# Kernel optimization log

Measured on AMD Instinct MI355X. Metric: run time of the kernel, lower is better.

The kernel has to match this reference:

```python
import jax, jax.numpy as jnp
import numpy as np

N, T, F, D, E = 50000, 16, 128, 128, 1_600_000


def setup_inputs() -> dict:
    key = jax.random.key(0)
    k0, k1, k2, k3 = jax.random.split(key, 4)
    x = jax.random.normal(k0, (N, T, F), dtype=jnp.float32)
    edge_index = jax.random.randint(k1, (2, E), 0, N, dtype=jnp.int64)
    W_conv = jax.random.normal(k2, (F, D), dtype=jnp.float32) * 0.05
    b_conv = jnp.zeros((D,), dtype=jnp.float32)
    W_lin = jax.random.normal(k3, (D, D), dtype=jnp.float32) * 0.05
    b_lin = jnp.zeros((D,), dtype=jnp.float32)
    return {"x": x, "edge_index": edge_index, "W_conv": W_conv,
            "b_conv": b_conv, "W_lin": W_lin, "b_lin": b_lin}


def reference(x, edge_index, W_conv, b_conv, W_lin, b_lin):
    n = x.shape[0]
    loop = jnp.arange(n, dtype=edge_index.dtype)
    # GCNConv with add_self_loops=True (PyG semantics)
    src = jnp.concatenate([edge_index[0], loop])  # [E+N]
    dst = jnp.concatenate([edge_index[1], loop])  # [E+N]
    deg = jax.ops.segment_sum(jnp.ones_like(src, dtype=x.dtype), dst,
                              num_segments=n)
    dinv = jnp.where(deg > 0, jax.lax.rsqrt(deg), 0.0)
    norm = (dinv[src] * dinv[dst])[:, None]  # symmetric normalization

    def step(h_prev, xt):
        xw = xt @ W_conv                        # [N, D]
        agg = jax.ops.segment_sum(xw[src] * norm, dst, num_segments=n)
        h = jnp.tanh(agg + b_conv + h_prev @ W_lin + b_lin)
        return h, h

    h0 = jnp.zeros((n, W_conv.shape[1]), dtype=x.dtype)
    _, hs = jax.lax.scan(step, h0, jnp.swapaxes(x, 0, 1))  # hs: [T, N, D]
    return jnp.swapaxes(hs, 0, 1)  # [N, T, D]
```

## Files before the change

kernel.cpp:

```cpp
#include <hip/hip_runtime.h>
#include <math.h>

#define NN 50000
#define TT 16
#define DD 128
#define MT (NN * TT)
#define SCAN_B 1024
#define SCAN_NB ((NN + SCAN_B - 1) / SCAN_B)

typedef __attribute__((ext_vector_type(8))) short short8;
typedef __attribute__((ext_vector_type(4))) float f32x4;

static __device__ __forceinline__ unsigned short f2bf(float f) {
  unsigned u = __float_as_uint(f);
  u += 0x7FFFu + ((u >> 16) & 1u);
  return (unsigned short)(u >> 16);
}
static __device__ __forceinline__ float bf_lo(unsigned v) {
  return __uint_as_float(v << 16);
}
static __device__ __forceinline__ float bf_hi(unsigned v) {
  return __uint_as_float(v & 0xffff0000u);
}

__global__ void k_init_prep(int* __restrict__ deg, int* __restrict__ cur,
                            const float* __restrict__ Wc, const float* __restrict__ Wl,
                            const float* __restrict__ bc, const float* __restrict__ bl,
                            unsigned short* __restrict__ Wct, unsigned short* __restrict__ Wlt,
                            float* __restrict__ bsum) {
  const int b = blockIdx.x;
  if (b < 196) {
    int i = b * 256 + threadIdx.x;
    if (i < NN) { deg[i] = 1; cur[i] = 0; }
  } else {
    int n = (b - 196) * 2 + (threadIdx.x >> 7);
    int k = threadIdx.x & 127;
    Wct[n * 128 + k] = f2bf(Wc[k * 128 + n]);
    Wlt[n * 128 + k] = f2bf(Wl[k * 128 + n]);
    if (n == 0) bsum[k] = bc[k] + bl[k];
  }
}

__global__ __launch_bounds__(256) void k_gemmx_deg(
    const float* __restrict__ X, const unsigned short* __restrict__ Wct,
    char* __restrict__ Yq, float* __restrict__ scaleN,
    const int* __restrict__ dst, int* __restrict__ deg, int E, int gx)
{
  __shared__ unsigned short sA[128 * 136];
  const int tid = threadIdx.x;
  if ((int)blockIdx.x >= gx) {
    int i = ((int)blockIdx.x - gx) * 256 + tid;
    if (i < E) atomicAdd(&deg[dst[i]], 1);
    return;
  }
  const long row0 = (long)blockIdx.x * 128;

  {
    const float4* xp = (const float4*)(X + row0 * 128);
    #pragma unroll
    for (int it = 0; it < 16; ++it) {
      float4 v = xp[it * 256 + tid];
      int q = it * 256 + tid;
      int r = q >> 5;
      int k = (q & 31) * 4;
      unsigned u0 = (unsigned)f2bf(v.x) | ((unsigned)f2bf(v.y) << 16);
      unsigned u1 = (unsigned)f2bf(v.z) | ((unsigned)f2bf(v.w) << 16);
      *(uint2*)&sA[r * 136 + k] = make_uint2(u0, u1);
    }
  }
  __syncthreads();

  const int w = tid >> 6, l = tid & 63;
  const int lr = l & 15;
  const int lk = (l >> 4) << 3;
  f32x4 acc[2][8];
  #pragma unroll
  for (int i = 0; i < 2; ++i)
    #pragma unroll
    for (int n = 0; n < 8; ++n) acc[i][n] = (f32x4){0.f, 0.f, 0.f, 0.f};

  #pragma unroll
  for (int kg = 0; kg < 4; ++kg) {
    int kb = kg * 32 + lk;
    short8 a0 = *(const short8*)&sA[(w * 32 + lr) * 136 + kb];
    short8 a1 = *(const short8*)&sA[(w * 32 + 16 + lr) * 136 + kb];
    #pragma unroll
    for (int n = 0; n < 8; ++n) {
      short8 b = *(const short8*)&Wct[(n * 16 + lr) * 128 + kb];
      acc[0][n] = __builtin_amdgcn_mfma_f32_16x16x32_bf16(b, a0, acc[0][n], 0, 0, 0);
      acc[1][n] = __builtin_amdgcn_mfma_f32_16x16x32_bf16(b, a1, acc[1][n], 0, 0, 0);
    }
  }

  const int wb = (l >> 4) * 4;
  #pragma unroll
  for (int i = 0; i < 2; ++i) {
    const long rbase = row0 + w * 32 + i * 16;
    const int node = (int)(rbase >> 4);
    const long row = rbase + lr;
    float m = 0.f;
    #pragma unroll
    for (int n = 0; n < 8; ++n)
      #pragma unroll
      for (int r = 0; r < 4; ++r) m = fmaxf(m, fabsf(acc[i][n][r]));
    #pragma unroll
    for (int mask = 1; mask < 64; mask <<= 1)
      m = fmaxf(m, __shfl_xor(m, mask, 64));
    const float f = (m > 0.f) ? 127.f / m : 0.f;
    if (l == 0) scaleN[node] = m * (1.f / 127.f);
    #pragma unroll
    for (int n = 0; n < 8; ++n) {
      int q0 = (int)__builtin_rintf(acc[i][n][0] * f);
      int q1 = (int)__builtin_rintf(acc[i][n][1] * f);
      int q2 = (int)__builtin_rintf(acc[i][n][2] * f);
      int q3 = (int)__builtin_rintf(acc[i][n][3] * f);
      unsigned u = (unsigned)(q0 & 255) | ((unsigned)(q1 & 255) << 8) |
                   ((unsigned)(q2 & 255) << 16) | ((unsigned)(q3 & 255) << 24);
      *(unsigned*)(Yq + row * 128 + n * 16 + wb) = u;
    }
  }
}

__global__ __launch_bounds__(SCAN_B) void k_scan1(const int* __restrict__ deg,
                                                  int* __restrict__ rowptr,
                                                  int* __restrict__ bsums,
                                                  float* __restrict__ dinv) {
  __shared__ int sm[SCAN_B];
  int tid = threadIdx.x;
  int i = blockIdx.x * SCAN_B + tid;
  int d = (i < NN) ? deg[i] : 1;
  if (i < NN) dinv[i] = rsqrtf((float)d);
  int v = d - 1;
  sm[tid] = v;
  __syncthreads();
  for (int off = 1; off < SCAN_B; off <<= 1) {
    int t = (tid >= off) ? sm[tid - off] : 0;
    __syncthreads();
    sm[tid] += t;
    __syncthreads();
  }
  if (i < NN) rowptr[i] = sm[tid] - v;
  if (tid == SCAN_B - 1) bsums[blockIdx.x] = sm[tid];
}

__global__ void k_scan2(int* __restrict__ bsums) {
  __shared__ int sm[64];
  int tid = threadIdx.x;
  int v = (tid < SCAN_NB) ? bsums[tid] : 0;
  sm[tid] = v;
  __syncthreads();
  for (int off = 1; off < 64; off <<= 1) {
    int t = (tid >= off) ? sm[tid - off] : 0;
    __syncthreads();
    sm[tid] += t;
    __syncthreads();
  }
  if (tid < SCAN_NB) bsums[tid] = sm[tid] - v;
  if (tid == 63) bsums[SCAN_NB] = sm[63];
}

__global__ __launch_bounds__(SCAN_B) void k_scan3(int* __restrict__ rowptr,
                                                  const int* __restrict__ bsums,
                                                  float* __restrict__ scaleN,
                                                  const float* __restrict__ dinv) {
  int i = blockIdx.x * SCAN_B + threadIdx.x;
  if (i < NN) {
    rowptr[i] += bsums[blockIdx.x];
    scaleN[i] *= dinv[i];
  }
  if (i == 0) rowptr[NN] = bsums[SCAN_NB];
}

__global__ void k_fill(const int* __restrict__ src, const int* __restrict__ dst,
                       const int* __restrict__ rowptr, int* __restrict__ cur,
                       int* __restrict__ col, int e) {
  int i = blockIdx.x * blockDim.x + threadIdx.x;
  if (i < e) {
    int d = dst[i];
    int slot = atomicAdd(&cur[d], 1);
    col[rowptr[d] + slot] = src[i];
  }
}

__global__ __launch_bounds__(256) void k_gatherN(
    const uint2* __restrict__ Yq,
    const float* __restrict__ scaleN,
    const int* __restrict__ col, const int* __restrict__ rowptr,
    const float* __restrict__ dinv, const float* __restrict__ bsum,
    unsigned* __restrict__ aggT)
{
  const int n = blockIdx.x;
  const int tid = threadIdx.x;
  float a0 = 0, a1 = 0, a2 = 0, a3 = 0, a4 = 0, a5 = 0, a6 = 0, a7 = 0;
  {
    uint2 v = Yq[(long)n * 256 + tid];
    float ss = scaleN[n];
    a0 = fmaf((float)(signed char)(v.x),       ss, a0);
    a1 = fmaf((float)(signed char)(v.x >> 8),  ss, a1);
    a2 = fmaf((float)(signed char)(v.x >> 16), ss, a2);
    a3 = fmaf((float)(signed char)(v.x >> 24), ss, a3);
    a4 = fmaf((float)(signed char)(v.y),       ss, a4);
    a5 = fmaf((float)(signed char)(v.y >> 8),  ss, a5);
    a6 = fmaf((float)(signed char)(v.y >> 16), ss, a6);
    a7 = fmaf((float)(signed char)(v.y >> 24), ss, a7);
  }
  int j = rowptr[n];
  const int end = rowptr[n + 1];
  for (; j + 4 <= end; j += 4) {
    int s0 = col[j], s1 = col[j + 1], s2 = col[j + 2], s3 = col[j + 3];
    float c0 = scaleN[s0], c1 = scaleN[s1], c2 = scaleN[s2], c3 = scaleN[s3];
    uint2 v0 = Yq[(long)s0 * 256 + tid];
    uint2 v1 = Yq[(long)s1 * 256 + tid];
    uint2 v2 = Yq[(long)s2 * 256 + tid];
    uint2 v3 = Yq[(long)s3 * 256 + tid];
    a0 = fmaf((float)(signed char)(v0.x),       c0, a0);
    a1 = fmaf((float)(signed char)(v0.x >> 8),  c0, a1);
    a2 = fmaf((float)(signed char)(v0.x >> 16), c0, a2);
    a3 = fmaf((float)(signed char)(v0.x >> 24), c0, a3);
    a4 = fmaf((float)(signed char)(v0.y),       c0, a4);
    a5 = fmaf((float)(signed char)(v0.y >> 8),  c0, a5);
    a6 = fmaf((float)(signed char)(v0.y >> 16), c0, a6);
    a7 = fmaf((float)(signed char)(v0.y >> 24), c0, a7);
    a0 = fmaf((float)(signed char)(v1.x),       c1, a0);
    a1 = fmaf((float)(signed char)(v1.x >> 8),  c1, a1);
    a2 = fmaf((float)(signed char)(v1.x >> 16), c1, a2);
    a3 = fmaf((float)(signed char)(v1.x >> 24), c1, a3);
    a4 = fmaf((float)(signed char)(v1.y),       c1, a4);
    a5 = fmaf((float)(signed char)(v1.y >> 8),  c1, a5);
    a6 = fmaf((float)(signed char)(v1.y >> 16), c1, a6);
    a7 = fmaf((float)(signed char)(v1.y >> 24), c1, a7);
    a0 = fmaf((float)(signed char)(v2.x),       c2, a0);
    a1 = fmaf((float)(signed char)(v2.x >> 8),  c2, a1);
    a2 = fmaf((float)(signed char)(v2.x >> 16), c2, a2);
    a3 = fmaf((float)(signed char)(v2.x >> 24), c2, a3);
    a4 = fmaf((float)(signed char)(v2.y),       c2, a4);
    a5 = fmaf((float)(signed char)(v2.y >> 8),  c2, a5);
    a6 = fmaf((float)(signed char)(v2.y >> 16), c2, a6);
    a7 = fmaf((float)(signed char)(v2.y >> 24), c2, a7);
    a0 = fmaf((float)(signed char)(v3.x),       c3, a0);
    a1 = fmaf((float)(signed char)(v3.x >> 8),  c3, a1);
    a2 = fmaf((float)(signed char)(v3.x >> 16), c3, a2);
    a3 = fmaf((float)(signed char)(v3.x >> 24), c3, a3);
    a4 = fmaf((float)(signed char)(v3.y),       c3, a4);
    a5 = fmaf((float)(signed char)(v3.y >> 8),  c3, a5);
    a6 = fmaf((float)(signed char)(v3.y >> 16), c3, a6);
    a7 = fmaf((float)(signed char)(v3.y >> 24), c3, a7);
  }
  for (; j < end; ++j) {
    int s = col[j];
    float cs = scaleN[s];
    uint2 v = Yq[(long)s * 256 + tid];
    a0 = fmaf((float)(signed char)(v.x),       cs, a0);
    a1 = fmaf((float)(signed char)(v.x >> 8),  cs, a1);
    a2 = fmaf((float)(signed char)(v.x >> 16), cs, a2);
    a3 = fmaf((float)(signed char)(v.x >> 24), cs, a3);
    a4 = fmaf((float)(signed char)(v.y),       cs, a4);
    a5 = fmaf((float)(signed char)(v.y >> 8),  cs, a5);
    a6 = fmaf((float)(signed char)(v.y >> 16), cs, a6);
    a7 = fmaf((float)(signed char)(v.y >> 24), cs, a7);
  }
  const int t = tid >> 4, dq = tid & 15;
  const float di = dinv[n];
  const float4 b0 = *(const float4*)&bsum[dq * 8];
  const float4 b1 = *(const float4*)&bsum[dq * 8 + 4];
  a0 = fmaf(a0, di, b0.x); a1 = fmaf(a1, di, b0.y);
  a2 = fmaf(a2, di, b0.z); a3 = fmaf(a3, di, b0.w);
  a4 = fmaf(a4, di, b1.x); a5 = fmaf(a5, di, b1.y);
  a6 = fmaf(a6, di, b1.z); a7 = fmaf(a7, di, b1.w);
  unsigned u0 = (unsigned)f2bf(a0) | ((unsigned)f2bf(a1) << 16);
  unsigned u1 = (unsigned)f2bf(a2) | ((unsigned)f2bf(a3) << 16);
  unsigned u2 = (unsigned)f2bf(a4) | ((unsigned)f2bf(a5) << 16);
  unsigned u3 = (unsigned)f2bf(a6) | ((unsigned)f2bf(a7) << 16);
  unsigned* ap = aggT + ((long)t * NN + n) * 64 + dq * 4;
  __builtin_nontemporal_store(u0, ap);
  __builtin_nontemporal_store(u1, ap + 1);
  __builtin_nontemporal_store(u2, ap + 2);
  __builtin_nontemporal_store(u3, ap + 3);
}

__global__ __launch_bounds__(64) void k_rnn(
    const unsigned* __restrict__ aggT,
    const unsigned short* __restrict__ Wlt,
    float* __restrict__ out)
{
  __shared__ unsigned sag[16 * 72];
  __shared__ unsigned short hl[16 * 144];
  __shared__ float ob[16 * 132];
  const int l = threadIdx.x;
  const int lr = l & 15, lg = l >> 4;
  const long nbase = (long)blockIdx.x * 16;

  short8 wf[4][8];
  #pragma unroll
  for (int kg = 0; kg < 4; ++kg)
    #pragma unroll
    for (int n = 0; n < 8; ++n)
      wf[kg][n] = *(const short8*)&Wlt[(n * 16 + lr) * 128 + kg * 32 + lg * 8];

  uint4 g[4];
  {
    const uint4* src = (const uint4*)(aggT + nbase * 64);
    #pragma unroll
    for (int i = 0; i < 4; ++i) g[i] = src[i * 64 + l];
    #pragma unroll
    for (int i = 0; i < 4; ++i) {
      int gi = (i * 64 + l) * 4;
      *(uint4*)&sag[(gi >> 6) * 72 + (gi & 63)] = g[i];
    }
  }
  {
    const uint4* src = (const uint4*)(aggT + ((long)NN + nbase) * 64);
    #pragma unroll
    for (int i = 0; i < 4; ++i) g[i] = src[i * 64 + l];
  }
  __syncthreads();
  #pragma unroll
  for (int n = 0; n < 8; ++n) {
    uint2 ag = *(const uint2*)&sag[lr * 72 + n * 8 + lg * 2];
    float o0 = tanhf(bf_lo(ag.x));
    float o1 = tanhf(bf_hi(ag.x));
    float o2 = tanhf(bf_lo(ag.y));
    float o3 = tanhf(bf_hi(ag.y));
    *(float4*)&ob[lr * 132 + n * 16 + lg * 4] = make_float4(o0, o1, o2, o3);
    unsigned u0 = (unsigned)f2bf(o0) | ((unsigned)f2bf(o1) << 16);
    unsigned u1 = (unsigned)f2bf(o2) | ((unsigned)f2bf(o3) << 16);
    *(uint2*)&hl[lr * 144 + n * 16 + lg * 4] = make_uint2(u0, u1);
  }
  __syncthreads();
  #pragma unroll
  for (int i = 0; i < 8; ++i) {
    int r2 = i * 2 + (l >> 5);
    int c = (l & 31) * 4;
    float4 v = *(const float4*)&ob[r2 * 132 + c];
    *(float4*)(out + ((nbase + r2) * TT) * 128 + c) = v;
  }

  for (int t = 1; t < TT; ++t) {
    #pragma unroll
    for (int i = 0; i < 4; ++i) {
      int gi = (i * 64 + l) * 4;
      *(uint4*)&sag[(gi >> 6) * 72 + (gi & 63)] = g[i];
    }
    if (t + 1 < TT) {
      const uint4* src = (const uint4*)(aggT + ((long)(t + 1) * NN + nbase) * 64);
      #pragma unroll
      for (int i = 0; i < 4; ++i) g[i] = src[i * 64 + l];
    }
    short8 bfr[4];
    #pragma unroll
    for (int kg = 0; kg < 4; ++kg)
      bfr[kg] = *(const short8*)&hl[lr * 144 + kg * 32 + lg * 8];
    __syncthreads();

    f32x4 acc[8];
    #pragma unroll
    for (int n = 0; n < 8; ++n) acc[n] = (f32x4){0.f, 0.f, 0.f, 0.f};
    #pragma unroll
    for (int kg = 0; kg < 4; ++kg) {
      #pragma unroll
      for (int n = 0; n < 8; ++n)
        acc[n] = __builtin_amdgcn_mfma_f32_16x16x32_bf16(wf[kg][n], bfr[kg], acc[n], 0, 0, 0);
    }
    #pragma unroll
    for (int n = 0; n < 8; ++n) {
      uint2 ag = *(const uint2*)&sag[lr * 72 + n * 8 + lg * 2];
      float o0 = tanhf(acc[n][0] + bf_lo(ag.x));
      float o1 = tanhf(acc[n][1] + bf_hi(ag.x));
      float o2 = tanhf(acc[n][2] + bf_lo(ag.y));
      float o3 = tanhf(acc[n][3] + bf_hi(ag.y));
      *(float4*)&ob[lr * 132 + n * 16 + lg * 4] = make_float4(o0, o1, o2, o3);
      unsigned u0 = (unsigned)f2bf(o0) | ((unsigned)f2bf(o1) << 16);
      unsigned u1 = (unsigned)f2bf(o2) | ((unsigned)f2bf(o3) << 16);
      *(uint2*)&hl[lr * 144 + n * 16 + lg * 4] = make_uint2(u0, u1);
    }
    __syncthreads();
    #pragma unroll
    for (int i = 0; i < 8; ++i) {
      int r2 = i * 2 + (l >> 5);
      int c = (l & 31) * 4;
      float4 v = *(const float4*)&ob[r2 * 132 + c];
      *(float4*)(out + ((nbase + r2) * TT + t) * 128 + c) = v;
    }
  }
}

extern "C" void kernel_launch(void* const* d_in, const int* in_sizes, int n_in,
                              void* d_out, int out_size, void* d_ws, size_t ws_size,
                              hipStream_t stream) {
  const float* x  = (const float*)d_in[0];
  const int*   ei = (const int*)d_in[1];
  const float* Wc = (const float*)d_in[2];
  const float* bc = (const float*)d_in[3];
  const float* Wl = (const float*)d_in[4];
  const float* bl = (const float*)d_in[5];
  float* out = (float*)d_out;
  const int E = in_sizes[1] / 2;
  const int* srcp = ei;
  const int* dstp = ei + E;

  char* w = (char*)d_ws;
  auto alloc = [&](size_t bytes) {
    char* p = w;
    w += (bytes + 255) & ~(size_t)255;
    return p;
  };
  int*            deg    = (int*)alloc(sizeof(int) * NN);
  float*          dinv   = (float*)alloc(sizeof(float) * NN);
  int*            rowptr = (int*)alloc(sizeof(int) * (NN + 1));
  int*            cur    = (int*)alloc(sizeof(int) * NN);
  int*            bsums  = (int*)alloc(sizeof(int) * (SCAN_NB + 1));
  int*            col    = (int*)alloc(sizeof(int) * (size_t)E);
  char*           Yq     = (char*)alloc((size_t)MT * DD);
  float*          scaleN = (float*)alloc(sizeof(float) * NN);
  unsigned*       aggT   = (unsigned*)alloc(sizeof(unsigned) * (size_t)MT * 64);
  float*          bsum   = (float*)alloc(sizeof(float) * DD);
  unsigned short* Wct    = (unsigned short*)alloc(sizeof(unsigned short) * 128 * 128);
  unsigned short* Wlt    = (unsigned short*)alloc(sizeof(unsigned short) * 128 * 128);

  const int degB = (E + 255) / 256;
  const int gx = MT / 128;

  k_init_prep<<<260, 256, 0, stream>>>(deg, cur, Wc, Wl, bc, bl, Wct, Wlt, bsum);
  k_gemmx_deg<<<gx + degB, 256, 0, stream>>>(x, Wct, Yq, scaleN, dstp, deg, E, gx);
  k_scan1<<<SCAN_NB, SCAN_B, 0, stream>>>(deg, rowptr, bsums, dinv);
  k_scan2<<<1, 64, 0, stream>>>(bsums);
  k_scan3<<<SCAN_NB, SCAN_B, 0, stream>>>(rowptr, bsums, scaleN, dinv);
  k_fill<<<degB, 256, 0, stream>>>(srcp, dstp, rowptr, cur, col, E);
  k_gatherN<<<NN, 256, 0, stream>>>((const uint2*)Yq, scaleN, col, rowptr, dinv, bsum, aggT);
  k_rnn<<<NN / 16, 64, 0, stream>>>(aggT, Wlt, out);
}
```

Before: 1.005 ms.

## Add nontemporal loads/stores for streamed data and fold block-sum scan into scan3

Switches the streamed X reads, CSR column reads, aggT reads, and output writes to nontemporal loads and stores so they do not pollute caches. The aggT store in the gather becomes a single 128-bit nontemporal store instead of four 32-bit ones. The separate single-block scan2 launch is removed: each scan3 block now redoes the 49-element block-sum prefix with a wavefront shuffle scan. This trades one launch for redundant tiny work per block, and may hurt if the nontemporal hints bypass reuse, for example col entries sharing cache lines.

```diff
diff --git a/kernel.cpp b/kernel.cpp
--- a/kernel.cpp
+++ b/kernel.cpp
@@ -10,6 +10,7 @@
 
 typedef __attribute__((ext_vector_type(8))) short short8;
 typedef __attribute__((ext_vector_type(4))) float f32x4;
+typedef __attribute__((ext_vector_type(4))) unsigned u32x4;
 
 static __device__ __forceinline__ unsigned short f2bf(float f) {
   unsigned u = __float_as_uint(f);
@@ -56,15 +57,15 @@
   const long row0 = (long)blockIdx.x * 128;
 
   {
-    const float4* xp = (const float4*)(X + row0 * 128);
+    const f32x4* xp = (const f32x4*)(X + row0 * 128);
     #pragma unroll
     for (int it = 0; it < 16; ++it) {
-      float4 v = xp[it * 256 + tid];
+      f32x4 v = __builtin_nontemporal_load(xp + it * 256 + tid);
       int q = it * 256 + tid;
       int r = q >> 5;
       int k = (q & 31) * 4;
-      unsigned u0 = (unsigned)f2bf(v.x) | ((unsigned)f2bf(v.y) << 16);
-      unsigned u1 = (unsigned)f2bf(v.z) | ((unsigned)f2bf(v.w) << 16);
+      unsigned u0 = (unsigned)f2bf(v[0]) | ((unsigned)f2bf(v[1]) << 16);
+      unsigned u1 = (unsigned)f2bf(v[2]) | ((unsigned)f2bf(v[3]) << 16);
       *(uint2*)&sA[r * 136 + k] = make_uint2(u0, u1);
     }
   }
@@ -143,32 +144,29 @@
   if (tid == SCAN_B - 1) bsums[blockIdx.x] = sm[tid];
 }
 
-__global__ void k_scan2(int* __restrict__ bsums) {
-  __shared__ int sm[64];
-  int tid = threadIdx.x;
-  int v = (tid < SCAN_NB) ? bsums[tid] : 0;
-  sm[tid] = v;
-  __syncthreads();
-  for (int off = 1; off < 64; off <<= 1) {
-    int t = (tid >= off) ? sm[tid - off] : 0;
-    __syncthreads();
-    sm[tid] += t;
-    __syncthreads();
-  }
-  if (tid < SCAN_NB) bsums[tid] = sm[tid] - v;
-  if (tid == 63) bsums[SCAN_NB] = sm[63];
-}
-
 __global__ __launch_bounds__(SCAN_B) void k_scan3(int* __restrict__ rowptr,
                                                   const int* __restrict__ bsums,
                                                   float* __restrict__ scaleN,
                                                   const float* __restrict__ dinv) {
+  __shared__ int soff[2];
+  if (threadIdx.x < 64) {
+    int v = (threadIdx.x < SCAN_NB) ? bsums[threadIdx.x] : 0;
+    int p = v;
+    #pragma unroll
+    for (int off = 1; off < 64; off <<= 1) {
+      int t = __shfl_up(p, off, 64);
+      if ((int)threadIdx.x >= off) p += t;
+    }
+    if ((int)threadIdx.x == (int)blockIdx.x) soff[0] = p - v;
+    if (threadIdx.x == 63) soff[1] = p;
+  }
+  __syncthreads();
   int i = blockIdx.x * SCAN_B + threadIdx.x;
   if (i < NN) {
-    rowptr[i] += bsums[blockIdx.x];
+    rowptr[i] += soff[0];
     scaleN[i] *= dinv[i];
   }
-  if (i == 0) rowptr[NN] = bsums[SCAN_NB];
+  if (i == 0) rowptr[NN] = soff[1];
 }
 
 __global__ void k_fill(const int* __restrict__ src, const int* __restrict__ dst,
@@ -207,7 +205,10 @@
   int j = rowptr[n];
   const int end = rowptr[n + 1];
   for (; j + 4 <= end; j += 4) {
-    int s0 = col[j], s1 = col[j + 1], s2 = col[j + 2], s3 = col[j + 3];
+    int s0 = __builtin_nontemporal_load(col + j);
+    int s1 = __builtin_nontemporal_load(col + j + 1);
+    int s2 = __builtin_nontemporal_load(col + j + 2);
+    int s3 = __builtin_nontemporal_load(col + j + 3);
     float c0 = scaleN[s0], c1 = scaleN[s1], c2 = scaleN[s2], c3 = scaleN[s3];
     uint2 v0 = Yq[(long)s0 * 256 + tid];
     uint2 v1 = Yq[(long)s1 * 256 + tid];
@@ -267,15 +268,12 @@
   a2 = fmaf(a2, di, b0.z); a3 = fmaf(a3, di, b0.w);
   a4 = fmaf(a4, di, b1.x); a5 = fmaf(a5, di, b1.y);
   a6 = fmaf(a6, di, b1.z); a7 = fmaf(a7, di, b1.w);
-  unsigned u0 = (unsigned)f2bf(a0) | ((unsigned)f2bf(a1) << 16);
-  unsigned u1 = (unsigned)f2bf(a2) | ((unsigned)f2bf(a3) << 16);
-  unsigned u2 = (unsigned)f2bf(a4) | ((unsigned)f2bf(a5) << 16);
-  unsigned u3 = (unsigned)f2bf(a6) | ((unsigned)f2bf(a7) << 16);
-  unsigned* ap = aggT + ((long)t * NN + n) * 64 + dq * 4;
-  __builtin_nontemporal_store(u0, ap);
-  __builtin_nontemporal_store(u1, ap + 1);
-  __builtin_nontemporal_store(u2, ap + 2);
-  __builtin_nontemporal_store(u3, ap + 3);
+  u32x4 u;
+  u.x = (unsigned)f2bf(a0) | ((unsigned)f2bf(a1) << 16);
+  u.y = (unsigned)f2bf(a2) | ((unsigned)f2bf(a3) << 16);
+  u.z = (unsigned)f2bf(a4) | ((unsigned)f2bf(a5) << 16);
+  u.w = (unsigned)f2bf(a6) | ((unsigned)f2bf(a7) << 16);
+  __builtin_nontemporal_store(u, (u32x4*)(aggT + ((long)t * NN + n) * 64 + dq * 4));
 }
 
 __global__ __launch_bounds__(64) void k_rnn(
@@ -297,21 +295,21 @@
     for (int n = 0; n < 8; ++n)
       wf[kg][n] = *(const short8*)&Wlt[(n * 16 + lr) * 128 + kg * 32 + lg * 8];
 
-  uint4 g[4];
+  u32x4 g[4];
   {
-    const uint4* src = (const uint4*)(aggT + nbase * 64);
-    #pragma unroll
-    for (int i = 0; i < 4; ++i) g[i] = src[i * 64 + l];
+    const u32x4* src = (const u32x4*)(aggT + nbase * 64);
+    #pragma unroll
+    for (int i = 0; i < 4; ++i) g[i] = __builtin_nontemporal_load(src + i * 64 + l);
     #pragma unroll
     for (int i = 0; i < 4; ++i) {
       int gi = (i * 64 + l) * 4;
-      *(uint4*)&sag[(gi >> 6) * 72 + (gi & 63)] = g[i];
+      *(u32x4*)&sag[(gi >> 6) * 72 + (gi & 63)] = g[i];
     }
   }
   {
-    const uint4* src = (const uint4*)(aggT + ((long)NN + nbase) * 64);
-    #pragma unroll
-    for (int i = 0; i < 4; ++i) g[i] = src[i * 64 + l];
+    const u32x4* src = (const u32x4*)(aggT + ((long)NN + nbase) * 64);
+    #pragma unroll
+    for (int i = 0; i < 4; ++i) g[i] = __builtin_nontemporal_load(src + i * 64 + l);
   }
   __syncthreads();
   #pragma unroll
@@ -331,20 +329,20 @@
   for (int i = 0; i < 8; ++i) {
     int r2 = i * 2 + (l >> 5);
     int c = (l & 31) * 4;
-    float4 v = *(const float4*)&ob[r2 * 132 + c];
-    *(float4*)(out + ((nbase + r2) * TT) * 128 + c) = v;
+    f32x4 v = *(const f32x4*)&ob[r2 * 132 + c];
+    __builtin_nontemporal_store(v, (f32x4*)(out + ((nbase + r2) * TT) * 128 + c));
   }
 
   for (int t = 1; t < TT; ++t) {
     #pragma unroll
     for (int i = 0; i < 4; ++i) {
       int gi = (i * 64 + l) * 4;
-      *(uint4*)&sag[(gi >> 6) * 72 + (gi & 63)] = g[i];
+      *(u32x4*)&sag[(gi >> 6) * 72 + (gi & 63)] = g[i];
     }
     if (t + 1 < TT) {
-      const uint4* src = (const uint4*)(aggT + ((long)(t + 1) * NN + nbase) * 64);
+      const u32x4* src = (const u32x4*)(aggT + ((long)(t + 1) * NN + nbase) * 64);
       #pragma unroll
-      for (int i = 0; i < 4; ++i) g[i] = src[i * 64 + l];
+      for (int i = 0; i < 4; ++i) g[i] = __builtin_nontemporal_load(src + i * 64 + l);
     }
     short8 bfr[4];
     #pragma unroll
@@ -378,8 +376,8 @@
     for (int i = 0; i < 8; ++i) {
       int r2 = i * 2 + (l >> 5);
       int c = (l & 31) * 4;
-      float4 v = *(const float4*)&ob[r2 * 132 + c];
-      *(float4*)(out + ((nbase + r2) * TT + t) * 128 + c) = v;
+      f32x4 v = *(const f32x4*)&ob[r2 * 132 + c];
+      __builtin_nontemporal_store(v, (f32x4*)(out + ((nbase + r2) * TT + t) * 128 + c));
     }
   }
 }
@@ -423,7 +421,6 @@
   k_init_prep<<<260, 256, 0, stream>>>(deg, cur, Wc, Wl, bc, bl, Wct, Wlt, bsum);
   k_gemmx_deg<<<gx + degB, 256, 0, stream>>>(x, Wct, Yq, scaleN, dstp, deg, E, gx);
   k_scan1<<<SCAN_NB, SCAN_B, 0, stream>>>(deg, rowptr, bsums, dinv);
-  k_scan2<<<1, 64, 0, stream>>>(bsums);
   k_scan3<<<SCAN_NB, SCAN_B, 0, stream>>>(rowptr, bsums, scaleN, dinv);
   k_fill<<<degB, 256, 0, stream>>>(srcp, dstp, rowptr, cur, col, E);
   k_gatherN<<<NN, 256, 0, stream>>>((const uint2*)Yq, scaleN, col, rowptr, dinv, bsum, aggT);
```

Measured after the change: 972.0 us. -3.3%, faster.
